# Kernel tuning notes

Measured on AMD Instinct MI355X. Metric: run time of the kernel, lower is better.

The kernel has to match this reference:

```python
import jax, jax.numpy as jnp
import numpy as np

EMB = 768
HEADS = 8
HEAD_DIM = EMB // HEADS
SCALE = HEAD_DIM ** -0.5


def setup_inputs() -> dict:
    key = jax.random.key(0)
    ks = jax.random.split(key, 9)
    s = 0.02
    return {
        "x": jax.random.normal(ks[0], (2, 4096, EMB), dtype=jnp.float32),
        "Wq": jax.random.normal(ks[1], (EMB, EMB), dtype=jnp.float32) * s,
        "bq": jax.random.normal(ks[2], (EMB,), dtype=jnp.float32) * s,
        "Wk": jax.random.normal(ks[3], (EMB, EMB), dtype=jnp.float32) * s,
        "bk": jax.random.normal(ks[4], (EMB,), dtype=jnp.float32) * s,
        "Wv": jax.random.normal(ks[5], (EMB, EMB), dtype=jnp.float32) * s,
        "bv": jax.random.normal(ks[6], (EMB,), dtype=jnp.float32) * s,
        "Wo": jax.random.normal(ks[7], (EMB, EMB), dtype=jnp.float32) * s,
        "bo": jax.random.normal(ks[8], (EMB,), dtype=jnp.float32) * s,
    }


def reference(x, Wq, bq, Wk, bk, Wv, bv, Wo, bo):
    b, n, _ = x.shape
    # torch Linear: y = x @ W.T + b
    def split_heads(y):  # [b, n, emb] -> [b, h, n, d]
        return y.reshape(b, n, HEADS, HEAD_DIM).transpose(0, 2, 1, 3)

    q = split_heads(x @ Wq.T + bq)
    k = split_heads(x @ Wk.T + bk)
    v = split_heads(x @ Wv.T + bv)
    # scores [b, h, q, k]; source applies scaling inside softmax input
    scores = jnp.einsum('bhqd,bhkd->bhqk', q, k) * SCALE
    weight = jax.nn.softmax(scores, axis=-1)
    out = jnp.einsum('bhqk,bhkd->bhqd', weight, v)
    out = out.transpose(0, 2, 1, 3).reshape(b, n, EMB)
    return out @ Wo.T + bo
```

## Files before the change

### kernel.cpp

```cpp
#include <hip/hip_runtime.h>


typedef __bf16 bf16;
typedef __attribute__((ext_vector_type(4))) float f32x4;
typedef __attribute__((ext_vector_type(16))) float f32x16;
typedef __attribute__((ext_vector_type(8))) __bf16 bf16x8;
typedef __attribute__((ext_vector_type(4))) __bf16 bf16x4;
typedef __attribute__((ext_vector_type(4))) unsigned u32x4;

#define EMB 768
#define SEQ 4096
#define NB 2
#define NHEADS 8
#define HD 96
#define BHTOT (NB * NHEADS)
#define MTOT (NB * SEQ)
#define QSCALE 0.14724241052735512f

__global__ __launch_bounds__(256) void cast_f32_bf16(const float* __restrict__ in,
                                                     bf16* __restrict__ out) {
  const int i = (blockIdx.x * 256 + threadIdx.x) * 4;
  const f32x4 v = *reinterpret_cast<const f32x4*>(in + i);
  bf16x4 o;
  o[0] = (bf16)v[0]; o[1] = (bf16)v[1]; o[2] = (bf16)v[2]; o[3] = (bf16)v[3];
  *reinterpret_cast<bf16x4*>(out + i) = o;
}

__global__ __launch_bounds__(256) void cast_w4(const float* __restrict__ w0,
                                               const float* __restrict__ w1,
                                               const float* __restrict__ w2,
                                               const float* __restrict__ w3,
                                               bf16* __restrict__ o0,
                                               bf16* __restrict__ o1,
                                               bf16* __restrict__ o2,
                                               bf16* __restrict__ o3) {
  const float* w = (blockIdx.y == 0) ? w0 : (blockIdx.y == 1) ? w1 : (blockIdx.y == 2) ? w2 : w3;
  bf16* o = (blockIdx.y == 0) ? o0 : (blockIdx.y == 1) ? o1 : (blockIdx.y == 2) ? o2 : o3;
  const int i = (blockIdx.x * 256 + threadIdx.x) * 4;
  const f32x4 v = *reinterpret_cast<const f32x4*>(w + i);
  bf16x4 ob;
  ob[0] = (bf16)v[0]; ob[1] = (bf16)v[1]; ob[2] = (bf16)v[2]; ob[3] = (bf16)v[3];
  *reinterpret_cast<bf16x4*>(o + i) = ob;
}

template <int MODE>
__global__ __launch_bounds__(256) void gemm_bt(const bf16* __restrict__ A,
                                               const bf16* __restrict__ B,
                                               const float* __restrict__ b0,
                                               const float* __restrict__ b1,
                                               const float* __restrict__ b2,
                                               void* __restrict__ out) {
  constexpr int K = EMB;
  __shared__ bf16 As[128 * 32];
  __shared__ bf16 Bs[128 * 32];
  const int tid = threadIdx.x;
  const int lane = tid & 63;
  const int wid = tid >> 6;
  const int wr = wid >> 1, wc = wid & 1;
  const int l15 = lane & 15, l4 = lane >> 4;
  const int rowBase = blockIdx.y * 128;
  const int colBase = blockIdx.x * 128;

  f32x4 acc[4][4] = {};

  for (int kt = 0; kt < K / 32; ++kt) {
    const int kb = kt * 32;
#pragma unroll
    for (int i = 0; i < 2; ++i) {
      const int c = (wid * 2 + i) * 64 + lane;
      const int row = c >> 2, cc = c & 3;
      const bf16* ga = A + (size_t)(rowBase + row) * K + kb + cc * 8;
      const bf16* gb = B + (size_t)(colBase + row) * K + kb + cc * 8;
      __builtin_amdgcn_global_load_lds(
          (const __attribute__((address_space(1))) void*)ga,
          (__attribute__((address_space(3))) void*)(As + (size_t)(wid * 2 + i) * 512),
          16, 0, 0);
      __builtin_amdgcn_global_load_lds(
          (const __attribute__((address_space(1))) void*)gb,
          (__attribute__((address_space(3))) void*)(Bs + (size_t)(wid * 2 + i) * 512),
          16, 0, 0);
    }
    __syncthreads();
    bf16x8 af[4], bfr[4];
#pragma unroll
    for (int t = 0; t < 4; ++t) {
      af[t]  = *reinterpret_cast<const bf16x8*>(As + (wr * 64 + t * 16 + l15) * 32 + l4 * 8);
      bfr[t] = *reinterpret_cast<const bf16x8*>(Bs + (wc * 64 + t * 16 + l15) * 32 + l4 * 8);
    }
#pragma unroll
    for (int mt = 0; mt < 4; ++mt)
#pragma unroll
      for (int nt = 0; nt < 4; ++nt)
        acc[mt][nt] = __builtin_amdgcn_mfma_f32_16x16x32_bf16(af[mt], bfr[nt], acc[mt][nt], 0, 0, 0);
    __syncthreads();
  }

#pragma unroll
  for (int mt = 0; mt < 4; ++mt) {
#pragma unroll
    for (int nt = 0; nt < 4; ++nt) {
      const int gn = colBase + wc * 64 + nt * 16 + l15;
      if (MODE == 0) {
        const int mm = gn / 768;
        const int g7 = gn - mm * 768;
        const int h = g7 / HD, d = g7 - h * HD;
        const float* bp = (mm == 0) ? b0 : (mm == 1) ? b1 : b2;
        const float bv = bp[g7];
        const float sc = (mm == 0) ? QSCALE : 1.f;
        bf16* dst = (bf16*)out + (size_t)mm * ((size_t)MTOT * EMB);
#pragma unroll
        for (int r = 0; r < 4; ++r) {
          const int gm = rowBase + wr * 64 + mt * 16 + l4 * 4 + r;
          const int b = gm >> 12, n = gm & (SEQ - 1);
          const float v = (acc[mt][nt][r] + bv) * sc;
          dst[((size_t)(b * NHEADS + h) * SEQ + n) * HD + d] = (bf16)v;
        }
      } else {
        const float bv = b0[gn];
#pragma unroll
        for (int r = 0; r < 4; ++r) {
          const int gm = rowBase + wr * 64 + mt * 16 + l4 * 4 + r;
          ((float*)out)[(size_t)gm * EMB + gn] = acc[mt][nt][r] + bv;
        }
      }
    }
  }
}

__global__ __launch_bounds__(256) void transpose_v(const bf16* __restrict__ v,
                                                   bf16* __restrict__ vt) {
  __shared__ bf16 T[96][72];
  const int bh = blockIdx.y;
  const int n0 = blockIdx.x * 64;
  const int tid = threadIdx.x;
#pragma unroll
  for (int i = 0; i < 3; ++i) {
    const int c = i * 256 + tid;
    const int n = c / 12, cc = c % 12;
    const bf16x8 val = *reinterpret_cast<const bf16x8*>(
        v + ((size_t)bh * SEQ + n0 + n) * HD + cc * 8);
#pragma unroll
    for (int j = 0; j < 8; ++j) T[cc * 8 + j][n] = val[j];
  }
  __syncthreads();
#pragma unroll
  for (int i = 0; i < 3; ++i) {
    const int c = i * 256 + tid;
    const int d = c >> 3, nc = c & 7;
    const int s0 = (nc >> 1) * 16 + (nc & 1) * 4;
    const bf16x4 lo = *reinterpret_cast<const bf16x4*>(&T[d][s0]);
    const bf16x4 hi = *reinterpret_cast<const bf16x4*>(&T[d][s0 + 8]);
    const bf16x8 val = __builtin_shufflevector(lo, hi, 0, 1, 2, 3, 4, 5, 6, 7);
    *reinterpret_cast<bf16x8*>(vt + ((size_t)bh * HD + d) * SEQ + n0 + nc * 8) = val;
  }
}

__global__ __launch_bounds__(256, 2) void attn_fwd(const bf16* __restrict__ q,
                                                   const bf16* __restrict__ k,
                                                   const bf16* __restrict__ vt,
                                                   bf16* __restrict__ o) {
  __shared__ bf16 Ks[2][64 * 128];
  __shared__ bf16 Vts[2][96 * 64];
  const int tid = threadIdx.x;
  const int lane = tid & 63;
  const int wid = tid >> 6;
  const int l31 = lane & 31, lhi = lane >> 5;
  const int bh = blockIdx.y;
  const int q0 = blockIdx.x * 128 + wid * 32;
  const size_t head = (size_t)bh * SEQ * HD;
  const bf16* kg = k + head;
  const bf16* vg = vt + (size_t)bh * (size_t)HD * SEQ;

  int kws[3], vws[3];
  const bf16* kgp[3];
  const bf16* vgp[3];
  const int vc = tid & 7;
#pragma unroll
  for (int i = 0; i < 3; ++i) {
    const int c = i * 256 + tid;
    const int kr = c / 12, kcc = c % 12;
    kws[i] = kr * 128 + ((kcc ^ (kr & 7)) * 8);
    kgp[i] = kg + (size_t)kr * HD + kcc * 8;
    const int vr = i * 32 + (tid >> 3);
    vws[i] = vr * 64 + ((vc ^ (vr & 7)) * 8);
    vgp[i] = vg + (size_t)vr * SEQ + vc * 8;
  }

  int krd[12], vrd[12];
#pragma unroll
  for (int kib = 0; kib < 2; ++kib)
#pragma unroll
    for (int dc = 0; dc < 6; ++dc) {
      const int row = kib * 32 + l31;
      krd[kib * 6 + dc] = (row * 128 + (((dc * 2 + lhi) ^ (l31 & 7)) * 8)) * 2;
    }
#pragma unroll
  for (int db = 0; db < 3; ++db)
#pragma unroll
    for (int kb = 0; kb < 4; ++kb) {
      const int row = db * 32 + l31;
      vrd[db * 4 + kb] = (row * 64 + (((kb * 2 + lhi) ^ (l31 & 7)) * 8)) * 2;
    }

  bf16x8 qf[6];
#pragma unroll
  for (int dc = 0; dc < 6; ++dc)
    qf[dc] = *reinterpret_cast<const bf16x8*>(
        q + head + (size_t)(q0 + l31) * HD + dc * 16 + lhi * 8);

  f32x16 oA = {}, oB = {}, oC = {};
  float lrun = 0.f;

#pragma unroll
  for (int i = 0; i < 3; ++i) {
    *reinterpret_cast<bf16x8*>(&Ks[0][kws[i]]) = *reinterpret_cast<const bf16x8*>(kgp[i]);
    *reinterpret_cast<bf16x8*>(&Vts[0][vws[i]]) = *reinterpret_cast<const bf16x8*>(vgp[i]);
  }
  __syncthreads();

  bf16x8 rk[3], rv[3];
  constexpr int NT = SEQ / 64;
  for (int kt = 0; kt < NT; ++kt) {
    const int cur = kt & 1;
    const bool pre = (kt < NT - 1);
    const char* ksb = (const char*)Ks[cur];
    const char* vsb = (const char*)Vts[cur];
    if (pre) {
      const size_t koff = (size_t)(kt + 1) * 64 * HD;
      const size_t voff = (size_t)(kt + 1) * 64;
#pragma unroll
      for (int i = 0; i < 3; ++i) {
        rk[i] = *reinterpret_cast<const bf16x8*>(kgp[i] + koff);
        rv[i] = *reinterpret_cast<const bf16x8*>(vgp[i] + voff);
      }
    }

    f32x16 s0 = {}, s1 = {};
    __builtin_amdgcn_s_setprio(1);
#pragma unroll
    for (int dc = 0; dc < 6; ++dc) {
      const bf16x8 kf0 = *reinterpret_cast<const bf16x8*>(ksb + krd[dc]);
      const bf16x8 kf1 = *reinterpret_cast<const bf16x8*>(ksb + krd[6 + dc]);
      s0 = __builtin_amdgcn_mfma_f32_32x32x16_bf16(kf0, qf[dc], s0, 0, 0, 0);
      s1 = __builtin_amdgcn_mfma_f32_32x32x16_bf16(kf1, qf[dc], s1, 0, 0, 0);
    }
    __builtin_amdgcn_s_setprio(0);

    float a0 = 0.f, a1 = 0.f, a2 = 0.f, a3 = 0.f;
#pragma unroll
    for (int i = 0; i < 4; ++i) {
      s0[4 * i + 0] = __builtin_amdgcn_exp2f(s0[4 * i + 0]); a0 += s0[4 * i + 0];
      s0[4 * i + 1] = __builtin_amdgcn_exp2f(s0[4 * i + 1]); a1 += s0[4 * i + 1];
      s0[4 * i + 2] = __builtin_amdgcn_exp2f(s0[4 * i + 2]); a2 += s0[4 * i + 2];
      s0[4 * i + 3] = __builtin_amdgcn_exp2f(s0[4 * i + 3]); a3 += s0[4 * i + 3];
    }
#pragma unroll
    for (int i = 0; i < 4; ++i) {
      s1[4 * i + 0] = __builtin_amdgcn_exp2f(s1[4 * i + 0]); a0 += s1[4 * i + 0];
      s1[4 * i + 1] = __builtin_amdgcn_exp2f(s1[4 * i + 1]); a1 += s1[4 * i + 1];
      s1[4 * i + 2] = __builtin_amdgcn_exp2f(s1[4 * i + 2]); a2 += s1[4 * i + 2];
      s1[4 * i + 3] = __builtin_amdgcn_exp2f(s1[4 * i + 3]); a3 += s1[4 * i + 3];
    }
    lrun += (a0 + a1) + (a2 + a3);

    bf16x8 pf[4];
#pragma unroll
    for (int blk = 0; blk < 2; ++blk) {
      const f32x16& s = blk ? s1 : s0;
      unsigned c[8];
#pragma unroll
      for (int i = 0; i < 8; ++i)
        asm("v_cvt_pk_bf16_f32 %0, %1, %2"
            : "=v"(c[i]) : "v"(s[2 * i]), "v"(s[2 * i + 1]));
      const u32x4 wa = {c[0], c[1], c[2], c[3]};
      const u32x4 wb = {c[4], c[5], c[6], c[7]};
      pf[blk * 2 + 0] = __builtin_bit_cast(bf16x8, wa);
      pf[blk * 2 + 1] = __builtin_bit_cast(bf16x8, wb);
    }

    __builtin_amdgcn_s_setprio(1);
#pragma unroll
    for (int kb = 0; kb < 4; ++kb) {
      const bf16x8 vf0 = *reinterpret_cast<const bf16x8*>(vsb + vrd[kb]);
      const bf16x8 vf1 = *reinterpret_cast<const bf16x8*>(vsb + vrd[4 + kb]);
      const bf16x8 vf2 = *reinterpret_cast<const bf16x8*>(vsb + vrd[8 + kb]);
      oA = __builtin_amdgcn_mfma_f32_32x32x16_bf16(vf0, pf[kb], oA, 0, 0, 0);
      oB = __builtin_amdgcn_mfma_f32_32x32x16_bf16(vf1, pf[kb], oB, 0, 0, 0);
      oC = __builtin_amdgcn_mfma_f32_32x32x16_bf16(vf2, pf[kb], oC, 0, 0, 0);
    }
    __builtin_amdgcn_s_setprio(0);

    if (pre) {
#pragma unroll
      for (int i = 0; i < 3; ++i) {
        *reinterpret_cast<bf16x8*>(&Ks[cur ^ 1][kws[i]]) = rk[i];
        *reinterpret_cast<bf16x8*>(&Vts[cur ^ 1][vws[i]]) = rv[i];
      }
    }
    __syncthreads();
  }

  lrun += __shfl_xor(lrun, 32, 64);
  const int n = q0 + l31;
  const int b = bh >> 3, h = bh & 7;
  bf16* obase = o + (size_t)(b * SEQ + n) * EMB + h * HD;
  const float inv = 1.f / lrun;
#pragma unroll
  for (int db = 0; db < 3; ++db) {
    const f32x16& ox = (db == 0) ? oA : (db == 1) ? oB : oC;
#pragma unroll
    for (int i = 0; i < 8; ++i) {
      const int r = 2 * i;
      const int d = db * 32 + (r & 3) + 8 * (r >> 2) + 4 * lhi;
      unsigned w;
      const float v0 = ox[r] * inv, v1 = ox[r + 1] * inv;
      asm("v_cvt_pk_bf16_f32 %0, %1, %2" : "=v"(w) : "v"(v0), "v"(v1));
      *reinterpret_cast<unsigned*>(obase + d) = w;
    }
  }
}

extern "C" void kernel_launch(void* const* d_in, const int* in_sizes, int n_in,
                              void* d_out, int out_size, void* d_ws, size_t ws_size,
                              hipStream_t stream) {
  const float* x  = (const float*)d_in[0];
  const float* Wq = (const float*)d_in[1];
  const float* bq = (const float*)d_in[2];
  const float* Wk = (const float*)d_in[3];
  const float* bk = (const float*)d_in[4];
  const float* Wv = (const float*)d_in[5];
  const float* bv = (const float*)d_in[6];
  const float* Wo = (const float*)d_in[7];
  const float* bo = (const float*)d_in[8];

  const size_t XN = (size_t)MTOT * EMB;
  const size_t WN = (size_t)EMB * EMB;

  bf16* p = (bf16*)d_ws;
  bf16* xbf = p; p += XN;
  bf16* wqb = p; p += WN;
  bf16* wkb = p; p += WN;
  bf16* wvb = p; p += WN;
  bf16* wob = p; p += WN;
  bf16* qb  = p; p += XN;
  bf16* kb  = p; p += XN;
  bf16* vb  = p; p += XN;
  bf16* vtb = p; p += XN;
  bf16* ao  = p; p += XN;

  cast_f32_bf16<<<XN / 1024, 256, 0, stream>>>(x, xbf);
  cast_w4<<<dim3(WN / 1024, 4), 256, 0, stream>>>(Wq, Wk, Wv, Wo, wqb, wkb, wvb, wob);

  gemm_bt<0><<<dim3(3 * EMB / 128, MTOT / 128), 256, 0, stream>>>(
      xbf, wqb, bq, bk, bv, qb);

  transpose_v<<<dim3(SEQ / 64, BHTOT), 256, 0, stream>>>(vb, vtb);

  attn_fwd<<<dim3(SEQ / 128, BHTOT), 256, 0, stream>>>(qb, kb, vtb, ao);

  gemm_bt<1><<<dim3(EMB / 128, MTOT / 128), 256, 0, stream>>>(ao, wob, bo, bo, bo, d_out);
}
```

Measured before the change: 208.0 us.

## Double queries per wave, pre-swizzle K/Vt in global, use direct global-to-LDS loads

The attention kernel now gives each wave 64 query rows instead of 32, so every K and V fragment read from LDS feeds two MFMAs, and it launches half as many blocks with a remapped block order. The QKV GEMM writes K into a padded 128-wide, XOR-swizzled layout, and the V transpose writes pre-swizzled columns. This lets the attention kernel fill LDS with async global_load_lds instead of going through registers and doing swizzled LDS stores. The cost is more accumulator registers per wave, which drops the two-blocks-per-CU launch bound, and a larger padded K buffer in the workspace.

```diff
diff --git a/kernel.cpp b/kernel.cpp
--- a/kernel.cpp
+++ b/kernel.cpp
@@ -16,6 +16,9 @@
 #define BHTOT (NB * NHEADS)
 #define MTOT (NB * SEQ)
 #define QSCALE 0.14724241052735512f
+
+#define AS1 __attribute__((address_space(1)))
+#define AS3 __attribute__((address_space(3)))
 
 __global__ __launch_bounds__(256) void cast_f32_bf16(const float* __restrict__ in,
                                                      bf16* __restrict__ out) {
@@ -49,7 +52,8 @@
                                                const float* __restrict__ b0,
                                                const float* __restrict__ b1,
                                                const float* __restrict__ b2,
-                                               void* __restrict__ out) {
+                                               void* __restrict__ out,
+                                               void* __restrict__ outK) {
   constexpr int K = EMB;
   __shared__ bf16 As[128 * 32];
   __shared__ bf16 Bs[128 * 32];
@@ -72,13 +76,11 @@
       const bf16* ga = A + (size_t)(rowBase + row) * K + kb + cc * 8;
       const bf16* gb = B + (size_t)(colBase + row) * K + kb + cc * 8;
       __builtin_amdgcn_global_load_lds(
-          (const __attribute__((address_space(1))) void*)ga,
-          (__attribute__((address_space(3))) void*)(As + (size_t)(wid * 2 + i) * 512),
-          16, 0, 0);
+          (const AS1 void*)ga,
+          (AS3 void*)(As + (size_t)(wid * 2 + i) * 512), 16, 0, 0);
       __builtin_amdgcn_global_load_lds(
-          (const __attribute__((address_space(1))) void*)gb,
-          (__attribute__((address_space(3))) void*)(Bs + (size_t)(wid * 2 + i) * 512),
-          16, 0, 0);
+          (const AS1 void*)gb,
+          (AS3 void*)(Bs + (size_t)(wid * 2 + i) * 512), 16, 0, 0);
     }
     __syncthreads();
     bf16x8 af[4], bfr[4];
@@ -107,13 +109,18 @@
         const float* bp = (mm == 0) ? b0 : (mm == 1) ? b1 : b2;
         const float bv = bp[g7];
         const float sc = (mm == 0) ? QSCALE : 1.f;
-        bf16* dst = (bf16*)out + (size_t)mm * ((size_t)MTOT * EMB);
 #pragma unroll
         for (int r = 0; r < 4; ++r) {
           const int gm = rowBase + wr * 64 + mt * 16 + l4 * 4 + r;
           const int b = gm >> 12, n = gm & (SEQ - 1);
           const float v = (acc[mt][nt][r] + bv) * sc;
-          dst[((size_t)(b * NHEADS + h) * SEQ + n) * HD + d] = (bf16)v;
+          if (mm == 1) {
+            ((bf16*)outK)[((size_t)(b * NHEADS + h) * SEQ + n) * 128 +
+                          (((d >> 3) ^ (n & 7)) << 3) + (d & 7)] = (bf16)v;
+          } else {
+            bf16* dst = (bf16*)out + (mm == 2 ? (size_t)MTOT * EMB : 0);
+            dst[((size_t)(b * NHEADS + h) * SEQ + n) * HD + d] = (bf16)v;
+          }
         }
       } else {
         const float bv = b0[gn];
@@ -147,44 +154,35 @@
   for (int i = 0; i < 3; ++i) {
     const int c = i * 256 + tid;
     const int d = c >> 3, nc = c & 7;
-    const int s0 = (nc >> 1) * 16 + (nc & 1) * 4;
-    const bf16x4 lo = *reinterpret_cast<const bf16x4*>(&T[d][s0]);
-    const bf16x4 hi = *reinterpret_cast<const bf16x4*>(&T[d][s0 + 8]);
+    const int s0i = (nc >> 1) * 16 + (nc & 1) * 4;
+    const bf16x4 lo = *reinterpret_cast<const bf16x4*>(&T[d][s0i]);
+    const bf16x4 hi = *reinterpret_cast<const bf16x4*>(&T[d][s0i + 8]);
     const bf16x8 val = __builtin_shufflevector(lo, hi, 0, 1, 2, 3, 4, 5, 6, 7);
-    *reinterpret_cast<bf16x8*>(vt + ((size_t)bh * HD + d) * SEQ + n0 + nc * 8) = val;
-  }
-}
-
-__global__ __launch_bounds__(256, 2) void attn_fwd(const bf16* __restrict__ q,
-                                                   const bf16* __restrict__ k,
-                                                   const bf16* __restrict__ vt,
-                                                   bf16* __restrict__ o) {
+    const int pc = nc ^ (d & 7);
+    *reinterpret_cast<bf16x8*>(vt + ((size_t)bh * HD + d) * SEQ + n0 + pc * 8) = val;
+  }
+}
+
+__global__ __launch_bounds__(256) void attn_fwd(const bf16* __restrict__ q,
+                                                const bf16* __restrict__ ksw,
+                                                const bf16* __restrict__ vt,
+                                                bf16* __restrict__ o) {
   __shared__ bf16 Ks[2][64 * 128];
   __shared__ bf16 Vts[2][96 * 64];
   const int tid = threadIdx.x;
   const int lane = tid & 63;
   const int wid = tid >> 6;
   const int l31 = lane & 31, lhi = lane >> 5;
-  const int bh = blockIdx.y;
-  const int q0 = blockIdx.x * 128 + wid * 32;
-  const size_t head = (size_t)bh * SEQ * HD;
-  const bf16* kg = k + head;
+  const int lin = blockIdx.y * 16 + blockIdx.x;
+  const int l2 = (lin & 7) * 32 + (lin >> 3);
+  const int qblk = l2 & 15, bh = l2 >> 4;
+  const int q0 = qblk * 256 + wid * 64;
+  const size_t headq = (size_t)bh * SEQ * HD;
+  const bf16* kg = ksw + (size_t)bh * SEQ * 128;
   const bf16* vg = vt + (size_t)bh * (size_t)HD * SEQ;
 
-  int kws[3], vws[3];
-  const bf16* kgp[3];
-  const bf16* vgp[3];
-  const int vc = tid & 7;
-#pragma unroll
-  for (int i = 0; i < 3; ++i) {
-    const int c = i * 256 + tid;
-    const int kr = c / 12, kcc = c % 12;
-    kws[i] = kr * 128 + ((kcc ^ (kr & 7)) * 8);
-    kgp[i] = kg + (size_t)kr * HD + kcc * 8;
-    const int vr = i * 32 + (tid >> 3);
-    vws[i] = vr * 64 + ((vc ^ (vr & 7)) * 8);
-    vgp[i] = vg + (size_t)vr * SEQ + vc * 8;
-  }
+  const bf16* kp = kg + (size_t)tid * 8;
+  const bf16* vp = vg + (size_t)(tid >> 3) * SEQ + (tid & 7) * 8;
 
   int krd[12], vrd[12];
 #pragma unroll
@@ -202,120 +200,116 @@
       vrd[db * 4 + kb] = (row * 64 + (((kb * 2 + lhi) ^ (l31 & 7)) * 8)) * 2;
     }
 
-  bf16x8 qf[6];
-#pragma unroll
-  for (int dc = 0; dc < 6; ++dc)
-    qf[dc] = *reinterpret_cast<const bf16x8*>(
-        q + head + (size_t)(q0 + l31) * HD + dc * 16 + lhi * 8);
-
-  f32x16 oA = {}, oB = {}, oC = {};
-  float lrun = 0.f;
-
-#pragma unroll
-  for (int i = 0; i < 3; ++i) {
-    *reinterpret_cast<bf16x8*>(&Ks[0][kws[i]]) = *reinterpret_cast<const bf16x8*>(kgp[i]);
-    *reinterpret_cast<bf16x8*>(&Vts[0][vws[i]]) = *reinterpret_cast<const bf16x8*>(vgp[i]);
-  }
+  bf16x8 qf[2][6];
+#pragma unroll
+  for (int g = 0; g < 2; ++g)
+#pragma unroll
+    for (int dc = 0; dc < 6; ++dc)
+      qf[g][dc] = *reinterpret_cast<const bf16x8*>(
+          q + headq + (size_t)(q0 + g * 32 + l31) * HD + dc * 16 + lhi * 8);
+
+  f32x16 oacc[2][3] = {};
+  float lrun[2] = {0.f, 0.f};
+
+#pragma unroll
+  for (int i = 0; i < 4; ++i)
+    __builtin_amdgcn_global_load_lds((const AS1 void*)(kp + i * 2048),
+                                     (AS3 void*)(&Ks[0][i * 2048 + wid * 512]), 16, 0, 0);
+#pragma unroll
+  for (int i = 0; i < 3; ++i)
+    __builtin_amdgcn_global_load_lds((const AS1 void*)(vp + (size_t)i * 131072),
+                                     (AS3 void*)(&Vts[0][i * 2048 + wid * 512]), 16, 0, 0);
+  kp += 8192;
+  vp += 64;
   __syncthreads();
 
-  bf16x8 rk[3], rv[3];
   constexpr int NT = SEQ / 64;
   for (int kt = 0; kt < NT; ++kt) {
     const int cur = kt & 1;
-    const bool pre = (kt < NT - 1);
+    if (kt < NT - 1) {
+#pragma unroll
+      for (int i = 0; i < 4; ++i)
+        __builtin_amdgcn_global_load_lds((const AS1 void*)(kp + i * 2048),
+                                         (AS3 void*)(&Ks[cur ^ 1][i * 2048 + wid * 512]), 16, 0, 0);
+#pragma unroll
+      for (int i = 0; i < 3; ++i)
+        __builtin_amdgcn_global_load_lds((const AS1 void*)(vp + (size_t)i * 131072),
+                                         (AS3 void*)(&Vts[cur ^ 1][i * 2048 + wid * 512]), 16, 0, 0);
+      kp += 8192;
+      vp += 64;
+    }
     const char* ksb = (const char*)Ks[cur];
     const char* vsb = (const char*)Vts[cur];
-    if (pre) {
-      const size_t koff = (size_t)(kt + 1) * 64 * HD;
-      const size_t voff = (size_t)(kt + 1) * 64;
-#pragma unroll
-      for (int i = 0; i < 3; ++i) {
-        rk[i] = *reinterpret_cast<const bf16x8*>(kgp[i] + koff);
-        rv[i] = *reinterpret_cast<const bf16x8*>(vgp[i] + voff);
-      }
-    }
-
-    f32x16 s0 = {}, s1 = {};
+
+    bf16x8 pf[2][4];
+#pragma unroll
+    for (int kib = 0; kib < 2; ++kib) {
+      f32x16 s[2] = {};
+      __builtin_amdgcn_s_setprio(1);
+#pragma unroll
+      for (int dc = 0; dc < 6; ++dc) {
+        const bf16x8 kf = *reinterpret_cast<const bf16x8*>(ksb + krd[kib * 6 + dc]);
+        s[0] = __builtin_amdgcn_mfma_f32_32x32x16_bf16(kf, qf[0][dc], s[0], 0, 0, 0);
+        s[1] = __builtin_amdgcn_mfma_f32_32x32x16_bf16(kf, qf[1][dc], s[1], 0, 0, 0);
+      }
+      __builtin_amdgcn_s_setprio(0);
+#pragma unroll
+      for (int g = 0; g < 2; ++g) {
+        float a0 = 0.f, a1 = 0.f, a2 = 0.f, a3 = 0.f;
+#pragma unroll
+        for (int i = 0; i < 4; ++i) {
+          s[g][4 * i + 0] = __builtin_amdgcn_exp2f(s[g][4 * i + 0]); a0 += s[g][4 * i + 0];
+          s[g][4 * i + 1] = __builtin_amdgcn_exp2f(s[g][4 * i + 1]); a1 += s[g][4 * i + 1];
+          s[g][4 * i + 2] = __builtin_amdgcn_exp2f(s[g][4 * i + 2]); a2 += s[g][4 * i + 2];
+          s[g][4 * i + 3] = __builtin_amdgcn_exp2f(s[g][4 * i + 3]); a3 += s[g][4 * i + 3];
+        }
+        lrun[g] += (a0 + a1) + (a2 + a3);
+        unsigned c[8];
+#pragma unroll
+        for (int i = 0; i < 8; ++i)
+          asm("v_cvt_pk_bf16_f32 %0, %1, %2"
+              : "=v"(c[i]) : "v"(s[g][2 * i]), "v"(s[g][2 * i + 1]));
+        const u32x4 wa = {c[0], c[1], c[2], c[3]};
+        const u32x4 wb = {c[4], c[5], c[6], c[7]};
+        pf[g][kib * 2 + 0] = __builtin_bit_cast(bf16x8, wa);
+        pf[g][kib * 2 + 1] = __builtin_bit_cast(bf16x8, wb);
+      }
+    }
+
     __builtin_amdgcn_s_setprio(1);
 #pragma unroll
-    for (int dc = 0; dc < 6; ++dc) {
-      const bf16x8 kf0 = *reinterpret_cast<const bf16x8*>(ksb + krd[dc]);
-      const bf16x8 kf1 = *reinterpret_cast<const bf16x8*>(ksb + krd[6 + dc]);
-      s0 = __builtin_amdgcn_mfma_f32_32x32x16_bf16(kf0, qf[dc], s0, 0, 0, 0);
-      s1 = __builtin_amdgcn_mfma_f32_32x32x16_bf16(kf1, qf[dc], s1, 0, 0, 0);
+    for (int kb = 0; kb < 4; ++kb) {
+#pragma unroll
+      for (int db = 0; db < 3; ++db) {
+        const bf16x8 vf = *reinterpret_cast<const bf16x8*>(vsb + vrd[db * 4 + kb]);
+        oacc[0][db] = __builtin_amdgcn_mfma_f32_32x32x16_bf16(vf, pf[0][kb], oacc[0][db], 0, 0, 0);
+        oacc[1][db] = __builtin_amdgcn_mfma_f32_32x32x16_bf16(vf, pf[1][kb], oacc[1][db], 0, 0, 0);
+      }
     }
     __builtin_amdgcn_s_setprio(0);
 
-    float a0 = 0.f, a1 = 0.f, a2 = 0.f, a3 = 0.f;
-#pragma unroll
-    for (int i = 0; i < 4; ++i) {
-      s0[4 * i + 0] = __builtin_amdgcn_exp2f(s0[4 * i + 0]); a0 += s0[4 * i + 0];
-      s0[4 * i + 1] = __builtin_amdgcn_exp2f(s0[4 * i + 1]); a1 += s0[4 * i + 1];
-      s0[4 * i + 2] = __builtin_amdgcn_exp2f(s0[4 * i + 2]); a2 += s0[4 * i + 2];
-      s0[4 * i + 3] = __builtin_amdgcn_exp2f(s0[4 * i + 3]); a3 += s0[4 * i + 3];
-    }
-#pragma unroll
-    for (int i = 0; i < 4; ++i) {
-      s1[4 * i + 0] = __builtin_amdgcn_exp2f(s1[4 * i + 0]); a0 += s1[4 * i + 0];
-      s1[4 * i + 1] = __builtin_amdgcn_exp2f(s1[4 * i + 1]); a1 += s1[4 * i + 1];
-      s1[4 * i + 2] = __builtin_amdgcn_exp2f(s1[4 * i + 2]); a2 += s1[4 * i + 2];
-      s1[4 * i + 3] = __builtin_amdgcn_exp2f(s1[4 * i + 3]); a3 += s1[4 * i + 3];
-    }
-    lrun += (a0 + a1) + (a2 + a3);
-
-    bf16x8 pf[4];
-#pragma unroll
-    for (int blk = 0; blk < 2; ++blk) {
-      const f32x16& s = blk ? s1 : s0;
-      unsigned c[8];
-#pragma unroll
-      for (int i = 0; i < 8; ++i)
-        asm("v_cvt_pk_bf16_f32 %0, %1, %2"
-            : "=v"(c[i]) : "v"(s[2 * i]), "v"(s[2 * i + 1]));
-      const u32x4 wa = {c[0], c[1], c[2], c[3]};
-      const u32x4 wb = {c[4], c[5], c[6], c[7]};
-      pf[blk * 2 + 0] = __builtin_bit_cast(bf16x8, wa);
-      pf[blk * 2 + 1] = __builtin_bit_cast(bf16x8, wb);
-    }
-
-    __builtin_amdgcn_s_setprio(1);
-#pragma unroll
-    for (int kb = 0; kb < 4; ++kb) {
-      const bf16x8 vf0 = *reinterpret_cast<const bf16x8*>(vsb + vrd[kb]);
-      const bf16x8 vf1 = *reinterpret_cast<const bf16x8*>(vsb + vrd[4 + kb]);
-      const bf16x8 vf2 = *reinterpret_cast<const bf16x8*>(vsb + vrd[8 + kb]);
-      oA = __builtin_amdgcn_mfma_f32_32x32x16_bf16(vf0, pf[kb], oA, 0, 0, 0);
-      oB = __builtin_amdgcn_mfma_f32_32x32x16_bf16(vf1, pf[kb], oB, 0, 0, 0);
-      oC = __builtin_amdgcn_mfma_f32_32x32x16_bf16(vf2, pf[kb], oC, 0, 0, 0);
-    }
-    __builtin_amdgcn_s_setprio(0);
-
-    if (pre) {
-#pragma unroll
-      for (int i = 0; i < 3; ++i) {
-        *reinterpret_cast<bf16x8*>(&Ks[cur ^ 1][kws[i]]) = rk[i];
-        *reinterpret_cast<bf16x8*>(&Vts[cur ^ 1][vws[i]]) = rv[i];
-      }
-    }
     __syncthreads();
   }
 
-  lrun += __shfl_xor(lrun, 32, 64);
-  const int n = q0 + l31;
   const int b = bh >> 3, h = bh & 7;
-  bf16* obase = o + (size_t)(b * SEQ + n) * EMB + h * HD;
-  const float inv = 1.f / lrun;
-#pragma unroll
-  for (int db = 0; db < 3; ++db) {
-    const f32x16& ox = (db == 0) ? oA : (db == 1) ? oB : oC;
-#pragma unroll
-    for (int i = 0; i < 8; ++i) {
-      const int r = 2 * i;
-      const int d = db * 32 + (r & 3) + 8 * (r >> 2) + 4 * lhi;
-      unsigned w;
-      const float v0 = ox[r] * inv, v1 = ox[r + 1] * inv;
-      asm("v_cvt_pk_bf16_f32 %0, %1, %2" : "=v"(w) : "v"(v0), "v"(v1));
-      *reinterpret_cast<unsigned*>(obase + d) = w;
+#pragma unroll
+  for (int g = 0; g < 2; ++g) {
+    float lr = lrun[g];
+    lr += __shfl_xor(lr, 32, 64);
+    const float inv = 1.f / lr;
+    const int n = q0 + g * 32 + l31;
+    bf16* obase = o + (size_t)(b * SEQ + n) * EMB + h * HD;
+#pragma unroll
+    for (int db = 0; db < 3; ++db) {
+#pragma unroll
+      for (int i = 0; i < 8; ++i) {
+        const int r = 2 * i;
+        const int d = db * 32 + (r & 3) + 8 * (r >> 2) + 4 * lhi;
+        unsigned w;
+        const float v0 = oacc[g][db][r] * inv, v1 = oacc[g][db][r + 1] * inv;
+        asm("v_cvt_pk_bf16_f32 %0, %1, %2" : "=v"(w) : "v"(v0), "v"(v1));
+        *reinterpret_cast<unsigned*>(obase + d) = w;
+      }
     }
   }
 }
@@ -335,28 +329,30 @@
 
   const size_t XN = (size_t)MTOT * EMB;
   const size_t WN = (size_t)EMB * EMB;
+  const size_t KSWN = (size_t)BHTOT * SEQ * 128;
 
   bf16* p = (bf16*)d_ws;
-  bf16* xbf = p; p += XN;
-  bf16* wqb = p; p += WN;
-  bf16* wkb = p; p += WN;
-  bf16* wvb = p; p += WN;
-  bf16* wob = p; p += WN;
-  bf16* qb  = p; p += XN;
-  bf16* kb  = p; p += XN;
-  bf16* vb  = p; p += XN;
-  bf16* vtb = p; p += XN;
-  bf16* ao  = p; p += XN;
+  bf16* xbf  = p; p += XN;
+  bf16* wqb  = p; p += WN;
+  bf16* wkb  = p; p += WN;
+  bf16* wvb  = p; p += WN;
+  bf16* wob  = p; p += WN;
+  bf16* qb   = p; p += XN;
+  bf16* vb   = p; p += XN;
+  bf16* kbsw = p; p += KSWN;
+  bf16* vtb  = p; p += XN;
+  bf16* ao   = p; p += XN;
 
   cast_f32_bf16<<<XN / 1024, 256, 0, stream>>>(x, xbf);
   cast_w4<<<dim3(WN / 1024, 4), 256, 0, stream>>>(Wq, Wk, Wv, Wo, wqb, wkb, wvb, wob);
 
   gemm_bt<0><<<dim3(3 * EMB / 128, MTOT / 128), 256, 0, stream>>>(
-      xbf, wqb, bq, bk, bv, qb);
+      xbf, wqb, bq, bk, bv, qb, kbsw);
 
   transpose_v<<<dim3(SEQ / 64, BHTOT), 256, 0, stream>>>(vb, vtb);
 
-  attn_fwd<<<dim3(SEQ / 128, BHTOT), 256, 0, stream>>>(qb, kb, vtb, ao);
-
-  gemm_bt<1><<<dim3(EMB / 128, MTOT / 128), 256, 0, stream>>>(ao, wob, bo, bo, bo, d_out);
-}
+  attn_fwd<<<dim3(SEQ / 256, BHTOT), 256, 0, stream>>>(qb, kbsw, vtb, ao);
+
+  gemm_bt<1><<<dim3(EMB / 128, MTOT / 128), 256, 0, stream>>>(
+      ao, wob, bo, nullptr, nullptr, d_out, nullptr);
+}
```

Result: slower. 237.3 us (+14.1%).
